# Kernel optimization log

Hardware: AMD Instinct MI355X
Metric: run time of the kernel (lower is better)

The kernel has to match this reference:

```python
import jax, jax.numpy as jnp
import numpy as np

ALPHA = 0.9  # smoothing coefficient from init_kwargs


def setup_inputs() -> dict:
    key = jax.random.key(0)
    x = jax.random.normal(key, (8, 4096, 1024), dtype=jnp.float32)
    return {"x": x}


def reference(x):
    # EMA along time axis (dim=1): y_t = alpha*y_{t-1} + (1-alpha)*x_t, y_{-1}=0
    alpha = jnp.asarray(ALPHA, dtype=x.dtype)
    om_alpha = jnp.asarray(1.0 - ALPHA, dtype=x.dtype)
    xt = jnp.swapaxes(x, 0, 1)  # [T, B, F]

    def step(carry, xt_t):
        y = alpha * carry + om_alpha * xt_t
        return y, y

    y0 = jnp.zeros(xt.shape[1:], dtype=x.dtype)  # [B, F]
    _, ys = jax.lax.scan(step, y0, xt)  # ys: [T, B, F]
    return jnp.swapaxes(ys, 0, 1)  # [B, T, F]
```

## Files before the change

kernel.cpp:

```cpp
#include <hip/hip_runtime.h>


using f4 = __attribute__((ext_vector_type(4))) float;

constexpr int Bn = 8;
constexpr int Tn = 4096;
constexpr int F4 = 256;
constexpr int L  = 128;
constexpr int W  = 64;
constexpr int P  = 16;
constexpr float A   = 0.9f;
constexpr float OMA = 0.1f;

template <int NSKIP, int NSTORE>
__device__ __forceinline__ void ema_stream(const f4* __restrict__ xs,
                                           f4* __restrict__ ys,
                                           float& ax, float& ay,
                                           float& az, float& aw) {
    constexpr int N = NSKIP + NSTORE;
    f4 buf[P];
    #pragma unroll
    for (int i = 0; i < P; ++i) buf[i] = xs[(size_t)i * F4];
    #pragma unroll
    for (int i = 0; i < N; ++i) {
        f4 v = buf[i % P];
        if (i + P < N) buf[i % P] = xs[(size_t)(i + P) * F4];
        ax = fmaf(A, ax, OMA * v.x);
        ay = fmaf(A, ay, OMA * v.y);
        az = fmaf(A, az, OMA * v.z);
        aw = fmaf(A, aw, OMA * v.w);
        if (i >= NSKIP) {
            f4 o;
            o.x = ax; o.y = ay; o.z = az; o.w = aw;
            __builtin_nontemporal_store(o, ys + (size_t)(i - NSKIP) * F4);
        }
        if ((i & 7) == 7) __builtin_amdgcn_s_barrier();
    }
}

__global__ __launch_bounds__(256) void ema_kernel(const f4* __restrict__ x,
                                                  f4* __restrict__ y) {
    const int blk  = blockIdx.x;
    const int xcd  = blk & 7;
    const int idx  = blk >> 3;
    const int g    = idx & 3;
    const int b    = idx >> 2;
    const int chunk = (xcd << 2) | g;
    const int t0    = chunk * L;

    const int f4i = threadIdx.x;

    const f4* __restrict__ xp = x + (size_t)b * Tn * F4 + f4i;
    f4*       __restrict__ yp = y + (size_t)b * Tn * F4 + f4i;

    float ax = 0.f, ay = 0.f, az = 0.f, aw = 0.f;
    f4* __restrict__ op = yp + (size_t)t0 * F4;

    if (chunk > 0) {
        ema_stream<W, L>(xp + (size_t)(t0 - W) * F4, op, ax, ay, az, aw);
    } else {
        ema_stream<0, L>(xp, op, ax, ay, az, aw);
    }
}

extern "C" void kernel_launch(void* const* d_in, const int* in_sizes, int n_in,
                              void* d_out, int out_size, void* d_ws, size_t ws_size,
                              hipStream_t stream) {
    const f4* x = (const f4*)d_in[0];
    f4*       y = (f4*)d_out;
    dim3 grid(Bn * (Tn / L));
    dim3 block(256);
    ema_kernel<<<grid, block, 0, stream>>>(x, y);
}
```

Before: 243.9 us.

## Split blocks into single-wave blocks and double-buffer loads in ping-pong batches

```diff
diff --git a/kernel.cpp b/kernel.cpp
--- a/kernel.cpp
+++ b/kernel.cpp
@@ -8,7 +8,7 @@
 constexpr int F4 = 256;
 constexpr int L  = 128;
 constexpr int W  = 64;
-constexpr int P  = 16;
+constexpr int PB = 8;
 constexpr float A   = 0.9f;
 constexpr float OMA = 0.1f;
 
@@ -17,38 +17,78 @@
                                            f4* __restrict__ ys,
                                            float& ax, float& ay,
                                            float& az, float& aw) {
-    constexpr int N = NSKIP + NSTORE;
-    f4 buf[P];
+    constexpr int N  = NSKIP + NSTORE;
+    constexpr int NB = N / PB;
+    static_assert(N % PB == 0 && NB % 2 == 0, "geometry");
+    f4 bufA[PB], bufB[PB];
+
     #pragma unroll
-    for (int i = 0; i < P; ++i) buf[i] = xs[(size_t)i * F4];
+    for (int i = 0; i < PB; ++i) bufA[i] = xs[(size_t)i * F4];
+    __builtin_amdgcn_sched_barrier(0);
+
     #pragma unroll
-    for (int i = 0; i < N; ++i) {
-        f4 v = buf[i % P];
-        if (i + P < N) buf[i % P] = xs[(size_t)(i + P) * F4];
-        ax = fmaf(A, ax, OMA * v.x);
-        ay = fmaf(A, ay, OMA * v.y);
-        az = fmaf(A, az, OMA * v.z);
-        aw = fmaf(A, aw, OMA * v.w);
-        if (i >= NSKIP) {
-            f4 o;
-            o.x = ax; o.y = ay; o.z = az; o.w = aw;
-            __builtin_nontemporal_store(o, ys + (size_t)(i - NSKIP) * F4);
+    for (int kb = 0; kb < NB; kb += 2) {
+        if (kb + 1 < NB) {
+            #pragma unroll
+            for (int i = 0; i < PB; ++i)
+                bufB[i] = xs[(size_t)((kb + 1) * PB + i) * F4];
         }
-        if ((i & 7) == 7) __builtin_amdgcn_s_barrier();
+        __builtin_amdgcn_sched_barrier(0);
+        #pragma unroll
+        for (int i = 0; i < PB; ++i) {
+            const int t = kb * PB + i;
+            f4 v = bufA[i];
+            ax = fmaf(A, ax, OMA * v.x);
+            ay = fmaf(A, ay, OMA * v.y);
+            az = fmaf(A, az, OMA * v.z);
+            aw = fmaf(A, aw, OMA * v.w);
+            if (t >= NSKIP) {
+                f4 o;
+                o.x = ax; o.y = ay; o.z = az; o.w = aw;
+                __builtin_nontemporal_store(o, ys + (size_t)(t - NSKIP) * F4);
+            }
+        }
+        __builtin_amdgcn_sched_barrier(0);
+        if (kb + 2 < NB) {
+            #pragma unroll
+            for (int i = 0; i < PB; ++i)
+                bufA[i] = xs[(size_t)((kb + 2) * PB + i) * F4];
+        }
+        __builtin_amdgcn_sched_barrier(0);
+        if (kb + 1 < NB) {
+            #pragma unroll
+            for (int i = 0; i < PB; ++i) {
+                const int t = (kb + 1) * PB + i;
+                f4 v = bufB[i];
+                ax = fmaf(A, ax, OMA * v.x);
+                ay = fmaf(A, ay, OMA * v.y);
+                az = fmaf(A, az, OMA * v.z);
+                aw = fmaf(A, aw, OMA * v.w);
+                if (t >= NSKIP) {
+                    f4 o;
+                    o.x = ax; o.y = ay; o.z = az; o.w = aw;
+                    __builtin_nontemporal_store(o, ys + (size_t)(t - NSKIP) * F4);
+                }
+            }
+        }
+        __builtin_amdgcn_sched_barrier(0);
     }
 }
 
-__global__ __launch_bounds__(256) void ema_kernel(const f4* __restrict__ x,
-                                                  f4* __restrict__ y) {
-    const int blk  = blockIdx.x;
-    const int xcd  = blk & 7;
-    const int idx  = blk >> 3;
-    const int g    = idx & 3;
-    const int b    = idx >> 2;
-    const int chunk = (xcd << 2) | g;
-    const int t0    = chunk * L;
+__global__ __launch_bounds__(64) void ema_kernel(const f4* __restrict__ x,
+                                                 f4* __restrict__ y) {
+    const int lane  = threadIdx.x;
+    const int blk   = blockIdx.x;
+    const int xcd   = blk & 7;
+    const int slot  = blk >> 3;
+    const int chunk = slot & 31;
+    const int phi   = slot >> 5;
+    const int p     = (phi << 3) | xcd;
+    const int fg    = p & 3;
+    const int b     = p >> 2;
 
-    const int f4i = threadIdx.x;
+    const int f4i = (fg << 6) | lane;
+    const int t0  = chunk * L;
 
     const f4* __restrict__ xp = x + (size_t)b * Tn * F4 + f4i;
     f4*       __restrict__ yp = y + (size_t)b * Tn * F4 + f4i;
@@ -68,7 +108,7 @@
                               hipStream_t stream) {
     const f4* x = (const f4*)d_in[0];
     f4*       y = (f4*)d_out;
-    dim3 grid(Bn * (Tn / L));
-    dim3 block(256);
+    dim3 grid(Bn * (Tn / L) * 4);
+    dim3 block(64);
     ema_kernel<<<grid, block, 0, stream>>>(x, y);
 }
```

Result: no change. 248.0 us (+1.7%).
